# Kernel tuning notes

Hardware: AMD Instinct MI355X
Metric: run time of the kernel (lower is better)

Reference implementation:

```python
import jax, jax.numpy as jnp
import numpy as np

K = 2          # hops
N_HEAD = 34    # relation types
H = 100        # hidden size
BS = 32
N_NODE = 200
EPS = 1e-20
INIT_RANGE = 0.01


def setup_inputs() -> dict:
    key = jax.random.key(0)
    ks = jax.random.split(key, 7)
    X = jax.random.normal(ks[0], (BS, N_NODE, H), dtype=jnp.float32)
    A = (jax.random.uniform(ks[1], (BS, N_HEAD, N_NODE, N_NODE)) < 0.05).astype(jnp.float32)
    start_attn = jax.random.uniform(ks[2], (BS, N_NODE), dtype=jnp.float32)
    end_attn = jax.random.uniform(ks[3], (BS, N_NODE), dtype=jnp.float32)
    uni_attn = jax.random.uniform(ks[4], (BS, N_HEAD), dtype=jnp.float32)
    trans_attn = jax.random.uniform(ks[5], (BS, N_HEAD, N_HEAD), dtype=jnp.float32)
    # dense branch: diag_decompose=False, n_basis=0 -> (k, n_head+1, h, h)
    w_vs = jax.random.uniform(ks[6], (K, N_HEAD + 1, H, H), dtype=jnp.float32,
                              minval=-INIT_RANGE, maxval=INIT_RANGE)
    return dict(X=X, A=A, start_attn=start_attn, end_attn=end_attn,
                uni_attn=uni_attn, trans_attn=trans_attn, w_vs=w_vs)


def reference(X, A, start_attn, end_attn, uni_attn, trans_attn, w_vs):
    # _get_weights (n_basis == 0, diag_decompose == False)
    W = w_vs[:, :-1]   # (k, n_head, h, h)
    Wi = w_vs[:, -1]   # (k, h, h)
    W_pad = [jnp.eye(H, dtype=X.dtype)]
    for t in range(K - 1):
        W_pad = [Wi[K - 1 - t] @ W_pad[0]] + W_pad   # length k

    # ---- Z propagation ----
    Z0 = X * start_attn[:, :, None]                  # (b, n, h)
    Z_all = []
    Zprev = None                                     # (b, f, n, h) after a hop
    for t in range(K):
        if t == 0:
            Zin = jnp.broadcast_to(Z0[:, :, :, None], (BS, N_NODE, H, N_HEAD))
        else:
            # permute + bmm with trans_attn: mix over incoming head f -> g
            Zin = jnp.einsum('bfni,bfg->bnig', Zprev, trans_attn)
        # per-head feature transform: (b,n,i,f) x (f,i,o) -> (b,f,n,o)
        Zh = jnp.einsum('bnif,fio->bfno', Zin, W[t])
        Zh = Zh * uni_attn[:, :, None, None]
        # adjacency propagation per head: A (b,f,m,n) x Z (b,f,n,o)
        Zh = jnp.einsum('bfmn,bfno->bfmo', A, Zh)    # (b, f, n, h)
        # sum heads, project with W_pad[t], gate by end_attn
        Zt = jnp.einsum('bfno,oi->bni', Zh, W_pad[t])
        Zt = Zt * end_attn[:, :, None]
        Z_all.append(Zt)
        Zprev = Zh

    # ---- degree normalizer D ----
    D_all = []
    Dprev = None                                     # (b, f, n)
    for t in range(K):
        if t == 0:
            Din = jnp.broadcast_to(start_attn[:, None, :], (BS, N_HEAD, N_NODE))
        else:
            Din = jnp.einsum('bfn,bfg->bgn', Dprev, trans_attn)
        Dh = Din * uni_attn[:, :, None]
        Dh = jnp.einsum('bfmn,bfn->bfm', A, Dh)      # (b, f, n)
        D_all.append(Dh.sum(axis=1) * end_attn)
        Dprev = Dh

    # per-hop outputs, normalized; stacked as (k, b, n, h)
    out = jnp.stack([Z / (D[:, :, None] + EPS) for Z, D in zip(Z_all, D_all)])
    return out
```

## Files before the change

kernel.cpp:

```cpp
#include <hip/hip_runtime.h>
#include <hip/hip_bf16.h>

#define NHEAD 34
#define HDIM  100
#define NNODE 200
#define NBATCH 32
#define EPSV 1e-20f

typedef __attribute__((ext_vector_type(8))) short bf16x8;
typedef __attribute__((ext_vector_type(4))) float f32x4;
typedef __attribute__((ext_vector_type(16))) float f32x16;
typedef __attribute__((ext_vector_type(4))) unsigned int ux4;

__device__ inline unsigned short bf16rne(float x) {
    unsigned u = __builtin_bit_cast(unsigned, x);
    unsigned r = (u + 0x7FFFu + ((u >> 16) & 1u)) >> 16;
    return (unsigned short)r;
}
__device__ inline float bf16tof(unsigned short h) {
    unsigned u = ((unsigned)h) << 16;
    return __builtin_bit_cast(float, u);
}

__device__ inline void split3_8(const float* v, bf16x8& p0, bf16x8& p1, bf16x8& p2) {
    #pragma unroll
    for (int j = 0; j < 8; j++) {
        float x = v[j];
        unsigned short h0 = bf16rne(x); float r1 = x - bf16tof(h0);
        unsigned short h1 = bf16rne(r1); float r2 = r1 - bf16tof(h1);
        unsigned short h2 = bf16rne(r2);
        p0[j] = (short)h0; p1[j] = (short)h1; p2[j] = (short)h2;
    }
}

__device__ inline void split2s(float x, unsigned short& h0, unsigned short& h1) {
    h0 = bf16rne(x);
    h1 = bf16rne(x - bf16tof(h0));
}
__device__ inline void split2_pack8(const float* v, bf16x8& a0, bf16x8& a1) {
    #pragma unroll
    for (int j = 0; j < 8; j++) {
        unsigned short h0, h1; split2s(v[j], h0, h1);
        a0[j] = (short)h0; a1[j] = (short)h1;
    }
}

__device__ inline bf16x8 afrag_bits(unsigned byte) {
    ux4 p;
    #pragma unroll
    for (int r = 0; r < 4; r++) {
        p[r] = ((byte >> (2 * r)) & 1u) * 0x3F80u + ((byte >> (2 * r + 1)) & 1u) * 0x3F800000u;
    }
    return __builtin_bit_cast(bf16x8, p);
}

__global__ __launch_bounds__(1024) void a_bitmask(const float* __restrict__ A,
                                                  unsigned long long* __restrict__ bm) {
    int row = blockIdx.x * 16 + (threadIdx.x >> 6);
    int lane = threadIdx.x & 63;
    if (row >= NBATCH * NHEAD * NNODE) return;
    const float* Ar = A + (size_t)row * NNODE;
    unsigned long long w0 = __ballot(Ar[lane] != 0.0f);
    unsigned long long w1 = __ballot(Ar[64 + lane] != 0.0f);
    unsigned long long w2 = __ballot(Ar[128 + lane] != 0.0f);
    unsigned long long w3 = __ballot(lane < 8 ? (Ar[192 + lane] != 0.0f) : false);
    if (lane == 0) {
        unsigned long long* p = bm + (size_t)row * 4;
        p[0] = w0; p[1] = w1; p[2] = w2; p[3] = w3;
    }
}

__global__ __launch_bounds__(256) void wsplit(const float* __restrict__ wv,
                                              short* __restrict__ wfr) {
    int fw = blockIdx.x;
    const float* W = wv + (size_t)(fw / 34) * 350000 + (size_t)(fw % 34) * 10000;
    for (int s0 = threadIdx.x; s0 < 28 * 64; s0 += 256) {
        int frag = s0 >> 6;
        int l = s0 & 63;
        int nt = frag >> 2, ks = frag & 3;
        int n = nt * 16 + (l & 15);
        int kb = ks * 32 + ((l >> 4) << 3);
        float v[8];
        #pragma unroll
        for (int j = 0; j < 8; j++) {
            int k = kb + j;
            v[j] = (k < 100 && n < 100) ? W[k * 100 + n] : 0.0f;
        }
        bf16x8 p0, p1, p2;
        split3_8(v, p0, p1, p2);
        size_t base = (((size_t)fw * 28 + frag) * 3) * 512 + l * 8;
        *(bf16x8*)&wfr[base]        = p0;
        *(bf16x8*)&wfr[base + 512]  = p1;
        *(bf16x8*)&wfr[base + 1024] = p2;
    }
}

__global__ __launch_bounds__(256) void asplit(const float* __restrict__ X,
                                              const float* __restrict__ start,
                                              short* __restrict__ xfr) {
    int b = blockIdx.x;
    const float* Xb = X + (size_t)b * 20000;
    const float* st = start + (size_t)b * NNODE;
    for (int s0 = threadIdx.x; s0 < 52 * 64; s0 += 256) {
        int frag = s0 >> 6;
        int l = s0 & 63;
        int mt = frag >> 2, ks = frag & 3;
        int row = mt * 16 + (l & 15);
        int kb = ks * 32 + ((l >> 4) << 3);
        float sc = (row < 200) ? st[row] : 0.0f;
        float v[8];
        #pragma unroll
        for (int j = 0; j < 8; j++) {
            int k = kb + j;
            v[j] = (row < 200 && k < 100) ? Xb[row * 100 + k] * sc : 0.0f;
        }
        bf16x8 p0, p1, p2;
        split3_8(v, p0, p1, p2);
        size_t base = (((size_t)b * 52 + frag) * 3) * 512 + l * 8;
        *(bf16x8*)&xfr[base]        = p0;
        *(bf16x8*)&xfr[base + 512]  = p1;
        *(bf16x8*)&xfr[base + 1024] = p2;
    }
}

template <int T>
__global__ __launch_bounds__(1024, 4) void fused_zha(
    const unsigned* __restrict__ bm32,
    const short* __restrict__ xfr,
    const float* __restrict__ Sfp,
    const short* __restrict__ wfr_t,
    const float* __restrict__ uni,
    const float* __restrict__ start,
    const float* __restrict__ dvec_g,
    float* __restrict__ Zout, float* __restrict__ Dh)
{
    int f = blockIdx.x, b = blockIdx.y;
    size_t bf = (size_t)b * NHEAD + f;
    int tid = threadIdx.x;
    int l = tid & 63, w = tid >> 6;

    __shared__ __align__(16) short zpl[2][128][216];
    __shared__ unsigned mkl[8][225];

    const unsigned* bmw = bm32 + bf * 1600;
    for (int idx = tid; idx < 1600; idx += 1024) mkl[idx & 7][idx >> 3] = bmw[idx];
    if (tid < 200) mkl[tid / 25][200 + tid % 25] = 0u;

    float u = uni[b * NHEAD + f];

    for (int idx = tid; idx < 28 * 216; idx += 1024) {
        int c = 100 + idx / 216, n = idx % 216;
        if (c == 100 && n < 200) continue;
        zpl[0][c][n] = 0; zpl[1][c][n] = 0;
    }
    if (tid < 200) {
        float dv;
        if constexpr (T == 0) dv = start[b * NNODE + tid] * u;
        else                  dv = dvec_g[bf * NNODE + tid];
        unsigned short h0, h1; split2s(dv, h0, h1);
        zpl[0][100][tid] = (short)h0; zpl[1][100][tid] = (short)h1;
    }

    const short* WF = wfr_t + (size_t)f * 28 * 3 * 512;
    for (int mt = w; mt < 13; mt += 16) {
        bf16x8 A0[4], A1[4];
        if constexpr (T == 0) {
            const short* AG = xfr + ((size_t)b * 52 + mt * 4) * 3 * 512;
            #pragma unroll
            for (int ks = 0; ks < 4; ks++) {
                A0[ks] = *(const bf16x8*)&AG[(ks * 3 + 0) * 512 + l * 8];
                A1[ks] = *(const bf16x8*)&AG[(ks * 3 + 1) * 512 + l * 8];
            }
        } else {
            const float* S = Sfp + bf * 20000;
            int row = mt * 16 + (l & 15);
            bool rok = row < 200;
            #pragma unroll
            for (int ks = 0; ks < 4; ks++) {
                int kb = ks * 32 + ((l >> 4) << 3);
                float4 z4 = make_float4(0.f, 0.f, 0.f, 0.f);
                float4 v0 = (rok && kb < 100)     ? *(const float4*)&S[row * 100 + kb]     : z4;
                float4 v1 = (rok && kb + 4 < 100) ? *(const float4*)&S[row * 100 + kb + 4] : z4;
                float vv[8] = {v0.x, v0.y, v0.z, v0.w, v1.x, v1.y, v1.z, v1.w};
                split2_pack8(vv, A0[ks], A1[ks]);
            }
        }
        for (int nt = 0; nt < 7; nt++) {
            f32x4 acc = {0.f, 0.f, 0.f, 0.f};
            #pragma unroll
            for (int ks = 0; ks < 4; ks++) {
                const short* wp = &WF[(size_t)((nt * 4 + ks) * 3) * 512 + l * 8];
                bf16x8 B0 = *(const bf16x8*)&wp[0];
                bf16x8 B1 = *(const bf16x8*)&wp[512];
                acc = __builtin_amdgcn_mfma_f32_16x16x32_bf16(A0[ks], B0, acc, 0, 0, 0);
                acc = __builtin_amdgcn_mfma_f32_16x16x32_bf16(A1[ks], B0, acc, 0, 0, 0);
                acc = __builtin_amdgcn_mfma_f32_16x16x32_bf16(A0[ks], B1, acc, 0, 0, 0);
            }
            int c = nt * 16 + (l & 15);
            if (c < 100) {
                int nb = mt * 16 + ((l >> 4) << 2);
                short4 q0, q1;
                #pragma unroll
                for (int r = 0; r < 4; r++) {
                    unsigned short h0, h1; split2s(acc[r] * u, h0, h1);
                    ((short*)&q0)[r] = (short)h0;
                    ((short*)&q1)[r] = (short)h1;
                }
                *(short4*)&zpl[0][c][nb] = q0;
                *(short4*)&zpl[1][c][nb] = q1;
            }
        }
    }
    __syncthreads();

    int cl = l & 31, kg = l >> 5;
    int mtg = w >> 2, ntg = w & 3;
    int nmt = (mtg < 3) ? 2 : 1;
    int myc = ntg * 32 + cl;

    f32x16 acc0, acc1;
    #pragma unroll
    for (int i = 0; i < 16; i++) { acc0[i] = 0.f; acc1[i] = 0.f; }

    for (int ks = 0; ks < 13; ks++) {
        bf16x8 z0 = *(const bf16x8*)&zpl[0][myc][ks * 16 + kg * 8];
        bf16x8 z1 = *(const bf16x8*)&zpl[1][myc][ks * 16 + kg * 8];
        int wq = ks >> 1;
        int shmt = ((ks & 1) << 4) | (kg << 3);
        #pragma unroll
        for (int mt = 0; mt < 2; mt++) {
            if (mt < nmt) {
                unsigned word = mkl[wq][(mtg * 2 + mt) * 32 + cl];
                bf16x8 af = afrag_bits((word >> shmt) & 0xFFu);
                f32x16* pa = mt ? &acc1 : &acc0;
                *pa = __builtin_amdgcn_mfma_f32_32x32x16_bf16(af, z0, *pa, 0, 0, 0);
                *pa = __builtin_amdgcn_mfma_f32_32x32x16_bf16(af, z1, *pa, 0, 0, 0);
            }
        }
    }

    __syncthreads();
    float* zs = (float*)&zpl[0][0][0];
    #pragma unroll
    for (int mt = 0; mt < 2; mt++) {
        if (mt < nmt && myc <= 100) {
            const f32x16& a = mt ? acc1 : acc0;
            int tb = (mtg * 2 + mt) * 32;
            #pragma unroll
            for (int r = 0; r < 16; r++) {
                int m = tb + (r & 3) + ((r >> 2) << 3) + (kg << 2);
                if (m < 200) zs[m * 104 + myc] = a[r];
            }
        }
    }
    __syncthreads();

    float* Zob = Zout + bf * 20000;
    float* Dhb = Dh + bf * NNODE;
    for (int idx = tid; idx < 200 * 26; idx += 1024) {
        int m = idx / 26, c4 = idx % 26;
        if (c4 < 25) *(float4*)&Zob[m * 100 + c4 * 4] = *(const float4*)&zs[m * 104 + c4 * 4];
        else Dhb[m] = zs[m * 104 + 100];
    }
}

__global__ __launch_bounds__(256) void zh_gemm(
    const float* __restrict__ src, const float* __restrict__ wbase,
    const float* __restrict__ uni, const float* __restrict__ rowscale,
    float* __restrict__ dst, int src_head)
{
    int f = blockIdx.x, b = blockIdx.y;
    int NHg = gridDim.x;
    const float* W = wbase + (size_t)f * 10000;
    const float* S = src + (size_t)(src_head ? (b * NHg + f) : b) * 20000;
    float* Dst = dst + (size_t)(b * NHg + f) * 20000;

    __shared__ __align__(16) float wl[10000];
    __shared__ __align__(16) float xl[5000];

    int tid = threadIdx.x;
    for (int idx = tid; idx < 10000; idx += 256) wl[idx] = W[idx];
    float u = uni ? uni[b * NHEAD + f] : 1.0f;

    int q = tid % 25;
    int ty = tid / 25;

    for (int c = 0; c < 4; c++) {
        __syncthreads();
        int base = c * 5000;
        for (int idx = tid; idx < 5000; idx += 256) {
            int row = idx / 100;
            float sc = rowscale ? rowscale[b * NNODE + c * 50 + row] : 1.0f;
            xl[idx] = S[base + idx] * sc;
        }
        __syncthreads();
        if (ty < 10) {
            float4 acc[5];
            #pragma unroll
            for (int r = 0; r < 5; r++) acc[r] = make_float4(0.f, 0.f, 0.f, 0.f);
            #pragma unroll 2
            for (int i = 0; i < 100; i++) {
                float4 w4 = *(const float4*)&wl[i * 100 + q * 4];
                #pragma unroll
                for (int r = 0; r < 5; r++) {
                    float x = xl[(ty + 10 * r) * 100 + i];
                    acc[r].x += x * w4.x; acc[r].y += x * w4.y;
                    acc[r].z += x * w4.z; acc[r].w += x * w4.w;
                }
            }
            #pragma unroll
            for (int r = 0; r < 5; r++) {
                int n = c * 50 + ty + 10 * r;
                float4 o4 = make_float4(acc[r].x * u, acc[r].y * u, acc[r].z * u, acc[r].w * u);
                *(float4*)&Dst[n * 100 + q * 4] = o4;
            }
        }
    }
}

__global__ void dmix_rs(const float* __restrict__ Dh0, const float* __restrict__ trans,
                        const float* __restrict__ uni, const float* __restrict__ endat,
                        float* __restrict__ dvec1, float* __restrict__ rs0) {
    int b = blockIdx.x;
    __shared__ float tl[NHEAD * NHEAD];
    for (int idx = threadIdx.x; idx < NHEAD * NHEAD; idx += 256) tl[idx] = trans[b * NHEAD * NHEAD + idx];
    __syncthreads();
    int n = threadIdx.x;
    if (n < NNODE) {
        float dh[NHEAD];
        float s = 0.f;
        #pragma unroll
        for (int f = 0; f < NHEAD; f++) { dh[f] = Dh0[((size_t)b * NHEAD + f) * NNODE + n]; s += dh[f]; }
        float e = endat[b * NNODE + n];
        rs0[b * NNODE + n] = e / (e * s + EPSV);
        #pragma unroll
        for (int g = 0; g < NHEAD; g++) {
            float acc = 0.f;
            #pragma unroll
            for (int f = 0; f < NHEAD; f++) acc += dh[f] * tl[f * NHEAD + g];
            dvec1[((size_t)b * NHEAD + g) * NNODE + n] = uni[b * NHEAD + g] * acc;
        }
    }
}

__global__ void dsum_rs(const float* __restrict__ Dh, const float* __restrict__ endat,
                        float* __restrict__ rs) {
    int idx = blockIdx.x * 256 + threadIdx.x;
    if (idx >= NBATCH * NNODE) return;
    int b = idx / NNODE, m = idx % NNODE;
    float s = 0.f;
    #pragma unroll
    for (int f = 0; f < NHEAD; f++) s += Dh[((size_t)b * NHEAD + f) * NNODE + m];
    float e = endat[idx];
    rs[idx] = e / (e * s + EPSV);
}

__global__ __launch_bounds__(256) void hmix(
    const float* __restrict__ Zsrc, const float* __restrict__ trans,
    float* __restrict__ Zdst, float* __restrict__ Zsum)
{
    int b = blockIdx.y;
    int c2 = blockIdx.x * 256 + threadIdx.x;
    __shared__ __align__(8) float tl[NHEAD * NHEAD];
    for (int idx = threadIdx.x; idx < NHEAD * NHEAD; idx += 256) tl[idx] = trans[b * NHEAD * NHEAD + idx];
    __syncthreads();
    if (c2 >= 10000) return;
    const float2* Zb = (const float2*)(Zsrc + (size_t)b * NHEAD * 20000) + c2;
    float2 acc[NHEAD];
    #pragma unroll
    for (int g = 0; g < NHEAD; g++) acc[g] = make_float2(0.f, 0.f);
    float2 s = make_float2(0.f, 0.f);
    for (int f = 0; f < NHEAD; f++) {
        float2 vf = Zb[(size_t)f * 10000];
        s.x += vf.x; s.y += vf.y;
        const float2* row = (const float2*)&tl[f * NHEAD];
        #pragma unroll
        for (int gq = 0; gq < 17; gq++) {
            float2 t2 = row[gq];
            acc[2 * gq].x     += vf.x * t2.x; acc[2 * gq].y     += vf.y * t2.x;
            acc[2 * gq + 1].x += vf.x * t2.y; acc[2 * gq + 1].y += vf.y * t2.y;
        }
    }
    ((float2*)(Zsum + (size_t)b * 20000))[c2] = s;
    float2* Zd = (float2*)(Zdst + (size_t)b * NHEAD * 20000) + c2;
    #pragma unroll
    for (int g = 0; g < NHEAD; g++) Zd[(size_t)g * 10000] = acc[g];
}

__global__ void fsum_out(const float* __restrict__ Zacc, const float* __restrict__ rs,
                         float* __restrict__ out) {
    int idx = blockIdx.x * 256 + threadIdx.x;
    if (idx >= NBATCH * 10000) return;
    int b = idx / 10000;
    int c2 = idx % 10000;
    const float2* Zb = (const float2*)(Zacc + (size_t)b * NHEAD * 20000) + c2;
    float2 s = make_float2(0.f, 0.f);
    #pragma unroll
    for (int g = 0; g < NHEAD; g++) {
        float2 v = Zb[(size_t)g * 10000];
        s.x += v.x; s.y += v.y;
    }
    int n = (c2 * 2) / 100;
    float r = rs[b * NNODE + n];
    s.x *= r; s.y *= r;
    ((float2*)out)[idx] = s;
}

extern "C" void kernel_launch(void* const* d_in, const int* in_sizes, int n_in,
                              void* d_out, int out_size, void* d_ws, size_t ws_size,
                              hipStream_t stream) {
    (void)in_sizes; (void)n_in;
    const float* X     = (const float*)d_in[0];
    const float* A     = (const float*)d_in[1];
    const float* start = (const float*)d_in[2];
    const float* endat = (const float*)d_in[3];
    const float* uni   = (const float*)d_in[4];
    const float* trans = (const float*)d_in[5];
    const float* wv    = (const float*)d_in[6];
    float* out = (float*)d_out;
    float* ws  = (float*)d_ws;

    size_t off = 0;
    unsigned long long* bm = (unsigned long long*)(ws); off += 1740800;
    float* buf1  = ws + off; off += 21760000;
    float* buf2  = ws + off; off += 21760000;
    float* Dh0   = ws + off; off += 217600;
    float* dvec1 = ws + off; off += 217600;
    float* Dh1   = ws + off; off += 217600;
    float* rs0   = ws + off; off += 6400;
    float* rs1   = ws + off; off += 6400;
    float* Zsum0 = ws + off; off += 640000;
    short* wfr   = (short*)(ws + off); off += 1462272;
    short* xfr   = (short*)(ws + off); off += 1277952;
    if (ws_size < off * sizeof(float)) {
        hipMemsetAsync(d_out, 0x7F, (size_t)out_size * sizeof(float), stream);
        return;
    }

    const float* Wi1 = wv + 690000;
    const short* wfr0 = wfr;
    const short* wfr1 = wfr + (size_t)34 * 28 * 3 * 512;
    const unsigned* bm32 = (const unsigned*)bm;

    dim3 gBF(NHEAD, NBATCH);

    a_bitmask<<<(NBATCH * NHEAD * NNODE + 15) / 16, 1024, 0, stream>>>(A, bm);
    wsplit<<<68, 256, 0, stream>>>(wv, wfr);
    asplit<<<32, 256, 0, stream>>>(X, start, xfr);

    fused_zha<0><<<gBF, 1024, 0, stream>>>(bm32, xfr, nullptr, wfr0, uni, start, nullptr, buf2, Dh0);
    dmix_rs<<<NBATCH, 256, 0, stream>>>(Dh0, trans, uni, endat, dvec1, rs0);
    hmix<<<dim3(40, NBATCH), 256, 0, stream>>>(buf2, trans, buf1, Zsum0);
    zh_gemm<<<dim3(1, NBATCH), 256, 0, stream>>>(Zsum0, Wi1, nullptr, rs0, out, 0);

    fused_zha<1><<<gBF, 1024, 0, stream>>>(bm32, nullptr, buf1, wfr1, uni, nullptr, dvec1, buf2, Dh1);
    dsum_rs<<<(NBATCH * NNODE + 255) / 256, 256, 0, stream>>>(Dh1, endat, rs1);
    fsum_out<<<(NBATCH * 10000 + 255) / 256, 256, 0, stream>>>(buf2, rs1, out + 640000);
}
```

Measured before the change: 382.3 us.

## Split fused_zha output columns across two blocks and parallelize the out0 GEMM

Each (batch, head) block of fused_zha is split into two blocks that each handle half of the output columns, with the degree column assigned to the second half. This halves LDS use per block and doubles the grid so more blocks can be resident and all CUs stay busy. The cost is that the bitmask load and the A-operand setup run twice per (batch, head). Separately, the hop-0 output projection GEMM now runs as four row-chunk blocks per batch instead of one serial loop, and the row scale is applied at the output rather than on load.

New measurement: 340.2 us. -11.0%, faster.

```diff
diff --git a/kernel.cpp b/kernel.cpp
--- a/kernel.cpp
+++ b/kernel.cpp
@@ -124,7 +124,7 @@
 }
 
 template <int T>
-__global__ __launch_bounds__(1024, 4) void fused_zha(
+__global__ __launch_bounds__(1024, 8) void fused_zha(
     const unsigned* __restrict__ bm32,
     const short* __restrict__ xfr,
     const float* __restrict__ Sfp,
@@ -134,12 +134,12 @@
     const float* __restrict__ dvec_g,
     float* __restrict__ Zout, float* __restrict__ Dh)
 {
-    int f = blockIdx.x, b = blockIdx.y;
+    int ch = blockIdx.x & 1, f = blockIdx.x >> 1, b = blockIdx.y;
     size_t bf = (size_t)b * NHEAD + f;
     int tid = threadIdx.x;
     int l = tid & 63, w = tid >> 6;
 
-    __shared__ __align__(16) short zpl[2][128][216];
+    __shared__ __align__(16) short zpl[2][64][216];
     __shared__ unsigned mkl[8][225];
 
     const unsigned* bmw = bm32 + bf * 1600;
@@ -148,20 +148,22 @@
 
     float u = uni[b * NHEAD + f];
 
-    for (int idx = tid; idx < 28 * 216; idx += 1024) {
-        int c = 100 + idx / 216, n = idx % 216;
-        if (c == 100 && n < 200) continue;
-        zpl[0][c][n] = 0; zpl[1][c][n] = 0;
-    }
-    if (tid < 200) {
-        float dv;
-        if constexpr (T == 0) dv = start[b * NNODE + tid] * u;
-        else                  dv = dvec_g[bf * NNODE + tid];
-        unsigned short h0, h1; split2s(dv, h0, h1);
-        zpl[0][100][tid] = (short)h0; zpl[1][100][tid] = (short)h1;
+    if (ch == 1) {
+        if (tid < 200) {
+            float dv;
+            if constexpr (T == 0) dv = start[b * NNODE + tid] * u;
+            else                  dv = dvec_g[bf * NNODE + tid];
+            unsigned short h0, h1; split2s(dv, h0, h1);
+            zpl[0][36][tid] = (short)h0; zpl[1][36][tid] = (short)h1;
+        } else if (tid < 232) {
+            int r = 200 + ((tid - 200) & 15), s = (tid - 200) >> 4;
+            zpl[s][36][r] = 0;
+        }
     }
 
     const short* WF = wfr_t + (size_t)f * 28 * 3 * 512;
+    int ntb = ch ? 4 : 0, nte = ch ? 7 : 4;
+    int coff = ch * 64;
     for (int mt = w; mt < 13; mt += 16) {
         bf16x8 A0[4], A1[4];
         if constexpr (T == 0) {
@@ -185,7 +187,7 @@
                 split2_pack8(vv, A0[ks], A1[ks]);
             }
         }
-        for (int nt = 0; nt < 7; nt++) {
+        for (int nt = ntb; nt < nte; nt++) {
             f32x4 acc = {0.f, 0.f, 0.f, 0.f};
             #pragma unroll
             for (int ks = 0; ks < 4; ks++) {
@@ -206,114 +208,103 @@
                     ((short*)&q0)[r] = (short)h0;
                     ((short*)&q1)[r] = (short)h1;
                 }
-                *(short4*)&zpl[0][c][nb] = q0;
-                *(short4*)&zpl[1][c][nb] = q1;
+                *(short4*)&zpl[0][c - coff][nb] = q0;
+                *(short4*)&zpl[1][c - coff][nb] = q1;
             }
         }
     }
     __syncthreads();
 
     int cl = l & 31, kg = l >> 5;
-    int mtg = w >> 2, ntg = w & 3;
-    int nmt = (mtg < 3) ? 2 : 1;
-    int myc = ntg * 32 + cl;
-
-    f32x16 acc0, acc1;
-    #pragma unroll
-    for (int i = 0; i < 16; i++) { acc0[i] = 0.f; acc1[i] = 0.f; }
-
-    for (int ks = 0; ks < 13; ks++) {
-        bf16x8 z0 = *(const bf16x8*)&zpl[0][myc][ks * 16 + kg * 8];
-        bf16x8 z1 = *(const bf16x8*)&zpl[1][myc][ks * 16 + kg * 8];
-        int wq = ks >> 1;
-        int shmt = ((ks & 1) << 4) | (kg << 3);
-        #pragma unroll
-        for (int mt = 0; mt < 2; mt++) {
-            if (mt < nmt) {
-                unsigned word = mkl[wq][(mtg * 2 + mt) * 32 + cl];
-                bf16x8 af = afrag_bits((word >> shmt) & 0xFFu);
-                f32x16* pa = mt ? &acc1 : &acc0;
-                *pa = __builtin_amdgcn_mfma_f32_32x32x16_bf16(af, z0, *pa, 0, 0, 0);
-                *pa = __builtin_amdgcn_mfma_f32_32x32x16_bf16(af, z1, *pa, 0, 0, 0);
-            }
-        }
-    }
-
-    __syncthreads();
+    int mt2 = w >> 1, cg = w & 1;
+    int myl = cg * 32 + cl;
+    bool act = (w < 14);
+
+    f32x16 acc2;
+    #pragma unroll
+    for (int i = 0; i < 16; i++) acc2[i] = 0.f;
+
+    if (act) {
+        for (int ks = 0; ks < 13; ks++) {
+            bf16x8 z0 = *(const bf16x8*)&zpl[0][myl][ks * 16 + kg * 8];
+            bf16x8 z1 = *(const bf16x8*)&zpl[1][myl][ks * 16 + kg * 8];
+            unsigned word = mkl[ks >> 1][mt2 * 32 + cl];
+            unsigned byte = (word >> (((ks & 1) << 4) | (kg << 3))) & 0xFFu;
+            bf16x8 af = afrag_bits(byte);
+            acc2 = __builtin_amdgcn_mfma_f32_32x32x16_bf16(af, z0, acc2, 0, 0, 0);
+            acc2 = __builtin_amdgcn_mfma_f32_32x32x16_bf16(af, z1, acc2, 0, 0, 0);
+        }
+    }
+    __syncthreads();
+
     float* zs = (float*)&zpl[0][0][0];
-    #pragma unroll
-    for (int mt = 0; mt < 2; mt++) {
-        if (mt < nmt && myc <= 100) {
-            const f32x16& a = mt ? acc1 : acc0;
-            int tb = (mtg * 2 + mt) * 32;
+    if (act) {
+        int myg = coff + myl;
+        if (myg <= 100) {
             #pragma unroll
             for (int r = 0; r < 16; r++) {
-                int m = tb + (r & 3) + ((r >> 2) << 3) + (kg << 2);
-                if (m < 200) zs[m * 104 + myc] = a[r];
+                int m = mt2 * 32 + (r & 3) + ((r >> 2) << 3) + (kg << 2);
+                if (m < 200) zs[m * 68 + myl] = acc2[r];
             }
         }
     }
     __syncthreads();
 
     float* Zob = Zout + bf * 20000;
-    float* Dhb = Dh + bf * NNODE;
-    for (int idx = tid; idx < 200 * 26; idx += 1024) {
-        int m = idx / 26, c4 = idx % 26;
-        if (c4 < 25) *(float4*)&Zob[m * 100 + c4 * 4] = *(const float4*)&zs[m * 104 + c4 * 4];
-        else Dhb[m] = zs[m * 104 + 100];
-    }
-}
-
-__global__ __launch_bounds__(256) void zh_gemm(
-    const float* __restrict__ src, const float* __restrict__ wbase,
-    const float* __restrict__ uni, const float* __restrict__ rowscale,
-    float* __restrict__ dst, int src_head)
+    if (ch == 0) {
+        for (int idx = tid; idx < 3200; idx += 1024) {
+            int m = idx >> 4, c4 = idx & 15;
+            *(float4*)&Zob[m * 100 + c4 * 4] = *(const float4*)&zs[m * 68 + c4 * 4];
+        }
+    } else {
+        float* Dhb = Dh + bf * NNODE;
+        for (int idx = tid; idx < 2000; idx += 1024) {
+            int m = idx / 10, c4 = idx % 10;
+            if (c4 < 9) *(float4*)&Zob[m * 100 + 64 + c4 * 4] = *(const float4*)&zs[m * 68 + c4 * 4];
+            else Dhb[m] = zs[m * 68 + 36];
+        }
+    }
+}
+
+__global__ __launch_bounds__(256) void out0_gemm(
+    const float* __restrict__ src, const float* __restrict__ W,
+    const float* __restrict__ rowscale, float* __restrict__ dst)
 {
-    int f = blockIdx.x, b = blockIdx.y;
-    int NHg = gridDim.x;
-    const float* W = wbase + (size_t)f * 10000;
-    const float* S = src + (size_t)(src_head ? (b * NHg + f) : b) * 20000;
-    float* Dst = dst + (size_t)(b * NHg + f) * 20000;
+    int c = blockIdx.x, b = blockIdx.y;
+    const float* S = src + (size_t)b * 20000;
+    float* Dst = dst + (size_t)b * 20000;
 
     __shared__ __align__(16) float wl[10000];
     __shared__ __align__(16) float xl[5000];
 
     int tid = threadIdx.x;
     for (int idx = tid; idx < 10000; idx += 256) wl[idx] = W[idx];
-    float u = uni ? uni[b * NHEAD + f] : 1.0f;
+    int base = c * 5000;
+    for (int idx = tid; idx < 5000; idx += 256) xl[idx] = S[base + idx];
+    __syncthreads();
 
     int q = tid % 25;
     int ty = tid / 25;
-
-    for (int c = 0; c < 4; c++) {
-        __syncthreads();
-        int base = c * 5000;
-        for (int idx = tid; idx < 5000; idx += 256) {
-            int row = idx / 100;
-            float sc = rowscale ? rowscale[b * NNODE + c * 50 + row] : 1.0f;
-            xl[idx] = S[base + idx] * sc;
-        }
-        __syncthreads();
-        if (ty < 10) {
-            float4 acc[5];
-            #pragma unroll
-            for (int r = 0; r < 5; r++) acc[r] = make_float4(0.f, 0.f, 0.f, 0.f);
-            #pragma unroll 2
-            for (int i = 0; i < 100; i++) {
-                float4 w4 = *(const float4*)&wl[i * 100 + q * 4];
-                #pragma unroll
-                for (int r = 0; r < 5; r++) {
-                    float x = xl[(ty + 10 * r) * 100 + i];
-                    acc[r].x += x * w4.x; acc[r].y += x * w4.y;
-                    acc[r].z += x * w4.z; acc[r].w += x * w4.w;
-                }
-            }
+    if (ty < 10) {
+        float4 acc[5];
+        #pragma unroll
+        for (int r = 0; r < 5; r++) acc[r] = make_float4(0.f, 0.f, 0.f, 0.f);
+        #pragma unroll 2
+        for (int i = 0; i < 100; i++) {
+            float4 w4 = *(const float4*)&wl[i * 100 + q * 4];
             #pragma unroll
             for (int r = 0; r < 5; r++) {
-                int n = c * 50 + ty + 10 * r;
-                float4 o4 = make_float4(acc[r].x * u, acc[r].y * u, acc[r].z * u, acc[r].w * u);
-                *(float4*)&Dst[n * 100 + q * 4] = o4;
-            }
+                float x = xl[(ty + 10 * r) * 100 + i];
+                acc[r].x += x * w4.x; acc[r].y += x * w4.y;
+                acc[r].z += x * w4.z; acc[r].w += x * w4.w;
+            }
+        }
+        #pragma unroll
+        for (int r = 0; r < 5; r++) {
+            int n = c * 50 + ty + 10 * r;
+            float sc = rowscale[b * NNODE + n];
+            float4 o4 = make_float4(acc[r].x * sc, acc[r].y * sc, acc[r].z * sc, acc[r].w * sc);
+            *(float4*)&Dst[n * 100 + q * 4] = o4;
         }
     }
 }
@@ -442,7 +433,7 @@
     const short* wfr1 = wfr + (size_t)34 * 28 * 3 * 512;
     const unsigned* bm32 = (const unsigned*)bm;
 
-    dim3 gBF(NHEAD, NBATCH);
+    dim3 gBF(NHEAD * 2, NBATCH);
 
     a_bitmask<<<(NBATCH * NHEAD * NNODE + 15) / 16, 1024, 0, stream>>>(A, bm);
     wsplit<<<68, 256, 0, stream>>>(wv, wfr);
@@ -451,7 +442,7 @@
     fused_zha<0><<<gBF, 1024, 0, stream>>>(bm32, xfr, nullptr, wfr0, uni, start, nullptr, buf2, Dh0);
     dmix_rs<<<NBATCH, 256, 0, stream>>>(Dh0, trans, uni, endat, dvec1, rs0);
     hmix<<<dim3(40, NBATCH), 256, 0, stream>>>(buf2, trans, buf1, Zsum0);
-    zh_gemm<<<dim3(1, NBATCH), 256, 0, stream>>>(Zsum0, Wi1, nullptr, rs0, out, 0);
+    out0_gemm<<<dim3(4, NBATCH), 256, 0, stream>>>(Zsum0, Wi1, rs0, out);
 
     fused_zha<1><<<gBF, 1024, 0, stream>>>(bm32, nullptr, buf1, wfr1, uni, nullptr, dvec1, buf2, Dh1);
     dsum_rs<<<(NBATCH * NNODE + 255) / 256, 256, 0, stream>>>(Dh1, endat, rs1);
```
